# Kernel tuning notes

Hardware: AMD Instinct MI355X
Metric: run time of the kernel (lower is better)

The kernel has to match this reference:

```python
import jax, jax.numpy as jnp
import numpy as np

DIM = 128
CODEBOOK_SIZE = 1024


def setup_inputs() -> dict:
    key = jax.random.key(0)
    kx, ke = jax.random.split(key)
    x = jax.random.normal(kx, (16, 4096, DIM), dtype=jnp.float32)
    # kaiming_uniform_ on (codebook_size, dim): bound = sqrt(6 / fan_in), fan_in = dim
    bound = float(np.sqrt(6.0 / DIM))
    embed = jax.random.uniform(ke, (CODEBOOK_SIZE, DIM), dtype=jnp.float32,
                               minval=-bound, maxval=bound)
    return {"x": x, "embed": embed}


def reference(x, embed):
    orig_shape = x.shape
    flat = x.reshape(-1, x.shape[-1])                     # [N, D]
    x2 = jnp.sum(flat * flat, axis=1, keepdims=True)      # [N, 1]
    e2 = jnp.sum(embed * embed, axis=1)                   # [K]
    dist = -(x2 - 2.0 * (flat @ embed.T) + e2[None, :])   # [N, K]
    embed_ind = jnp.argmax(dist, axis=-1)                 # [N]
    embed_ind = embed_ind.reshape(orig_shape[:-1])        # [B, S]
    quantize = jnp.take(embed, embed_ind, axis=0)         # [B, S, D]
    return quantize, embed_ind
```

## Files before the change

kernel.cpp:

```cpp
#include <hip/hip_runtime.h>

#define DIM     128
#define NCODES  1024
#define TILE_M  64
#define FLAGThr 0.018f
#define RPB     4
#define RGRID   1024

typedef __attribute__((ext_vector_type(8))) _Float16 half8;
typedef __attribute__((ext_vector_type(4))) _Float16 half4;
typedef __attribute__((ext_vector_type(4))) float    f32x4;

#define AS1 __attribute__((address_space(1)))
#define AS3 __attribute__((address_space(3)))


__global__ __launch_bounds__(256) void setup_kernel(
    const float* __restrict__ embed, double* __restrict__ e2d,
    float* __restrict__ e2f, _Float16* __restrict__ eh,
    float* __restrict__ embedT, int* __restrict__ cnt)
{
  __shared__ float tile[64][132];
  __shared__ double psum[4][64];
  if (blockIdx.x == 0 && threadIdx.x == 0) *cnt = 0;
  const int c0 = blockIdx.x * 64;
  const int t  = threadIdx.x;

  const f32x4* E4 = (const f32x4*)(embed + (size_t)c0 * DIM);
  #pragma unroll
  for (int i = 0; i < 8; ++i) {
    int e = t + i * 256;
    int r = e >> 5, c4 = e & 31;
    f32x4 v = E4[e];
    *(f32x4*)&tile[r][c4 * 4] = v;
    half4 h;
    h[0] = (_Float16)v[0]; h[1] = (_Float16)v[1];
    h[2] = (_Float16)v[2]; h[3] = (_Float16)v[3];
    *(half4*)&eh[(size_t)(c0 + r) * DIM + c4 * 4] = h;
  }
  __syncthreads();

  {
    int r = t & 63, part = t >> 6;
    double s = 0.0;
    #pragma unroll
    for (int k = 0; k < 32; ++k) {
      float v = tile[r][part * 32 + k];
      s += (double)v * v;
    }
    psum[part][r] = s;
  }
  __syncthreads();
  if (t < 64) {
    double s = psum[0][t] + psum[1][t] + psum[2][t] + psum[3][t];
    e2d[c0 + t] = s;
    e2f[c0 + t] = (float)s;
  }

  #pragma unroll
  for (int i = 0; i < 32; ++i) {
    int idx = t + i * 256;
    int k = idx >> 6, c = idx & 63;
    embedT[(size_t)k * NCODES + c0 + c] = tile[c][k];
  }
}

__global__ __launch_bounds__(256, 3) void pass1_kernel(
    const float* __restrict__ x, const float* __restrict__ embed,
    const _Float16* __restrict__ eh, const float* __restrict__ e2f,
    float* __restrict__ outQ, float* __restrict__ outIdx,
    int* __restrict__ cnt, int* __restrict__ list)
{
  __shared__ __align__(16) _Float16 xh[TILE_M * 136];
  __shared__ __align__(16) unsigned char bbuf[2][64 * 256];
  __shared__ float rb_best[4][TILE_M];
  __shared__ float rb_sec [4][TILE_M];
  __shared__ int   fidx[TILE_M];

  const int tid  = threadIdx.x;
  const int row0 = blockIdx.x * TILE_M;
  const int l  = tid & 63, w = tid >> 6;
  const int rl = l & 15,  q = l >> 4;

#define STAGE_B(CH, BUF)                                                      \
  {                                                                           \
    const char* ebase = (const char*)eh + (size_t)(CH) * 64 * 256;            \
    _Pragma("unroll")                                                         \
    for (int j = 0; j < 4; ++j) {                                             \
      int u  = (w * 4 + j) * 64 + l;              \
      int rr = u >> 4, cc = u & 15;                                           \
      const char* src = ebase + rr * 256 + ((cc ^ (rr & 15)) * 16);           \
      __builtin_amdgcn_global_load_lds(                                       \
          (AS1 void*)src,                                                     \
          (AS3 void*)((BUF) + (w * 4 + j) * 1024), 16, 0, 0);                 \
    }                                                                         \
  }

  {
    const f32x4* x4 = (const f32x4*)(x + (size_t)row0 * DIM);
    #pragma unroll
    for (int i = 0; i < 8; ++i) {
      int e = tid + i * 256;
      int r = e >> 5, c4 = e & 31;
      f32x4 v = x4[e];
      half4 h;
      h[0] = (_Float16)v[0]; h[1] = (_Float16)v[1];
      h[2] = (_Float16)v[2]; h[3] = (_Float16)v[3];
      *(half4*)&xh[r * 136 + c4 * 4] = h;
    }
  }
  STAGE_B(0, bbuf[0])
  __syncthreads();

  half8 afrag[4][4];
  #pragma unroll
  for (int m = 0; m < 4; ++m)
    #pragma unroll
    for (int ks = 0; ks < 4; ++ks)
      afrag[m][ks] = *(const half8*)&xh[(m * 16 + rl) * 136 + ks * 32 + q * 8];

  float bestp[16], secp[16];
  #pragma unroll
  for (int s = 0; s < 16; ++s) { bestp[s] = -3.0e38f; secp[s] = -3.3e38f; }

  #pragma unroll
  for (int ch = 0; ch < 16; ++ch) {
    if (ch < 15) STAGE_B(ch + 1, bbuf[(ch + 1) & 1])
    const unsigned char* bb = bbuf[ch & 1];
    half8 bfrag[4];
    #pragma unroll
    for (int ks = 0; ks < 4; ++ks)
      bfrag[ks] = *(const half8*)(bb + (w * 16 + rl) * 256 +
                                  (((ks * 4 + q) ^ rl) * 16));
    const float vinit = fmaf(-0.5f, e2f[ch * 64 + w * 16 + rl], -16.0f);
    const int mycode = ch * 64 + w * 16 + rl;
    #pragma unroll
    for (int m = 0; m < 4; ++m) {
      f32x4 acc = (f32x4){vinit, vinit, vinit, vinit};
      #pragma unroll
      for (int ks = 0; ks < 4; ++ks)
        acc = __builtin_amdgcn_mfma_f32_16x16x32_f16(afrag[m][ks], bfrag[ks], acc, 0, 0, 0);
      #pragma unroll
      for (int r = 0; r < 4; ++r) {
        const int s = m * 4 + r;
        float scp = __int_as_float((__float_as_int(acc[r]) & ~1023) | mycode);
        secp[s]  = __builtin_amdgcn_fmed3f(scp, bestp[s], secp[s]);
        bestp[s] = fmaxf(bestp[s], scp);
      }
    }
    __syncthreads();
  }
#undef STAGE_B

  #pragma unroll
  for (int off = 1; off < 16; off <<= 1) {
    #pragma unroll
    for (int s = 0; s < 16; ++s) {
      float ob = __shfl_xor(bestp[s], off, 16);
      float os = __shfl_xor(secp[s],  off, 16);
      secp[s]  = fmaxf(__builtin_amdgcn_fmed3f(bestp[s], ob, secp[s]), os);
      bestp[s] = fmaxf(bestp[s], ob);
    }
  }
  if (rl == 0) {
    #pragma unroll
    for (int m = 0; m < 4; ++m)
      #pragma unroll
      for (int r = 0; r < 4; ++r) {
        int s = m * 4 + r;
        int row = m * 16 + q * 4 + r;
        rb_best[w][row] = bestp[s];
        rb_sec [w][row] = secp[s];
      }
  }
  __syncthreads();

  if (tid < TILE_M) {
    float bv = rb_best[0][tid], sv = rb_sec[0][tid];
    #pragma unroll
    for (int ww = 1; ww < 4; ++ww) {
      float ob = rb_best[ww][tid], os = rb_sec[ww][tid];
      sv = fmaxf(__builtin_amdgcn_fmed3f(bv, ob, sv), os);
      bv = fmaxf(bv, ob);
    }
    int bi = __float_as_int(bv) & 1023;
    int grow = row0 + tid;
    outIdx[grow] = (float)bi;
    fidx[tid] = bi;
    if (bv - sv <= FLAGThr) {
      int p = atomicAdd(cnt, 1);
      list[p] = grow;
    }
  }
  __syncthreads();

  {
    const f32x4* E4   = (const f32x4*)embed;
    f32x4*       out4 = (f32x4*)(outQ + (size_t)row0 * DIM);
    #pragma unroll
    for (int i = 0; i < 8; ++i) {
      int e = tid + i * 256;
      int r = e >> 5, c4 = e & 31;
      out4[e] = E4[fidx[r] * 32 + c4];
    }
  }
}

__global__ __launch_bounds__(256) void refine2_kernel(
    const float* __restrict__ x, const float* __restrict__ embed,
    const float* __restrict__ embedT,
    const double* __restrict__ e2d, const float* __restrict__ e2f,
    float* __restrict__ outQ, float* __restrict__ outIdx,
    const int* __restrict__ cnt, const int* __restrict__ list)
{
  __shared__ f32x4 xst[DIM];
  __shared__ float rb1[RPB][4], rb2[RPB][4];
  __shared__ int   ri1[RPB][4], ri2[RPB][4];
  __shared__ int   cand[RPB][2];

  const int t = threadIdx.x;
  const int l = t & 63, w = t >> 6;
  const int n = *cnt;
  float* xsf = (float*)xst;

  for (int base = blockIdx.x * RPB; base < n; base += RGRID * RPB) {
    const int nr = min(RPB, n - base);
    #pragma unroll
    for (int i = 0; i < 2; ++i) {
      int idx = t + i * 256;
      int r = idx >> 7, k = idx & 127;
      float v = 0.f;
      if (r < nr) v = x[(size_t)list[base + r] * DIM + k];
      xsf[k * RPB + r] = v;
    }
    __syncthreads();

    f32x4 dot[RPB];
    #pragma unroll
    for (int r = 0; r < RPB; ++r) dot[r] = (f32x4){0.f, 0.f, 0.f, 0.f};
    const f32x4* eT4 = (const f32x4*)embedT;
    #pragma unroll 4
    for (int k = 0; k < DIM; ++k) {
      f32x4 e4  = eT4[k * 256 + t];
      f32x4 xk4 = xst[k];
      #pragma unroll
      for (int r = 0; r < RPB; ++r) {
        dot[r][0] = fmaf(xk4[r], e4[0], dot[r][0]);
        dot[r][1] = fmaf(xk4[r], e4[1], dot[r][1]);
        dot[r][2] = fmaf(xk4[r], e4[2], dot[r][2]);
        dot[r][3] = fmaf(xk4[r], e4[3], dot[r][3]);
      }
    }

    #pragma unroll
    for (int r = 0; r < RPB; ++r) {
      float b1 = 3.4e38f, b2 = 3.4e38f; int i1 = 0, i2 = 0;
      #pragma unroll
      for (int j = 0; j < 4; ++j) {
        int c = 4 * t + j;
        float sc = fmaf(-2.0f, dot[r][j], e2f[c]);
        bool better = (sc < b1);
        float lv = better ? b1 : sc;  int li = better ? i1 : c;
        if (better) { b1 = sc; i1 = c; }
        bool t2 = (lv < b2) || (lv == b2 && li < i2);
        if (t2) { b2 = lv; i2 = li; }
      }
      #pragma unroll
      for (int off = 1; off < 64; off <<= 1) {
        float o1 = __shfl_xor(b1, off, 64); int oi1 = __shfl_xor(i1, off, 64);
        float o2 = __shfl_xor(b2, off, 64); int oi2 = __shfl_xor(i2, off, 64);
        bool take = (o1 < b1) || (o1 == b1 && oi1 < i1);
        float n1 = take ? o1 : b1; int ni1 = take ? oi1 : i1;
        float lo = take ? b1 : o1; int loi = take ? i1 : oi1;
        float c2v = take ? o2 : b2; int c2i = take ? oi2 : i2;
        bool u2 = (c2v < lo) || (c2v == lo && c2i < loi);
        b1 = n1; i1 = ni1;
        b2 = u2 ? c2v : lo; i2 = u2 ? c2i : loi;
      }
      if (l == 0) { rb1[r][w] = b1; ri1[r][w] = i1; rb2[r][w] = b2; ri2[r][w] = i2; }
    }
    __syncthreads();

    if (t < RPB) {
      float v1 = rb1[t][0], v2 = rb2[t][0]; int j1 = ri1[t][0], j2 = ri2[t][0];
      #pragma unroll
      for (int ww = 1; ww < 4; ++ww) {
        float o1 = rb1[t][ww], o2 = rb2[t][ww]; int oi1 = ri1[t][ww], oi2 = ri2[t][ww];
        bool take = (o1 < v1) || (o1 == v1 && oi1 < j1);
        float n1 = take ? o1 : v1; int ni1 = take ? oi1 : j1;
        float lo = take ? v1 : o1; int loi = take ? j1 : oi1;
        float c2v = take ? o2 : v2; int c2i = take ? oi2 : j2;
        bool u2 = (c2v < lo) || (c2v == lo && c2i < loi);
        v1 = n1; j1 = ni1; v2 = u2 ? c2v : lo; j2 = u2 ? c2i : loi;
      }
      cand[t][0] = j1; cand[t][1] = j2;
    }
    __syncthreads();

    if (w < nr) {
      int c1 = cand[w][0], c2 = cand[w][1];
      float xa = xsf[l * RPB + w], xb = xsf[(l + 64) * RPB + w];
      double p1 = (double)xa * (double)embed[(size_t)c1 * DIM + l]
                + (double)xb * (double)embed[(size_t)c1 * DIM + 64 + l];
      double p2 = (double)xa * (double)embed[(size_t)c2 * DIM + l]
                + (double)xb * (double)embed[(size_t)c2 * DIM + 64 + l];
      #pragma unroll
      for (int off = 1; off < 64; off <<= 1) {
        p1 += __shfl_xor(p1, off, 64);
        p2 += __shfl_xor(p2, off, 64);
      }
      double s1 = e2d[c1] - 2.0 * p1;
      double s2 = e2d[c2] - 2.0 * p2;
      int widx = ((s2 < s1) || (s2 == s1 && c2 < c1)) ? c2 : c1;
      int row = list[base + w];
      if (l == 0) outIdx[row] = (float)widx;
      outQ[(size_t)row * DIM + l]      = embed[(size_t)widx * DIM + l];
      outQ[(size_t)row * DIM + 64 + l] = embed[(size_t)widx * DIM + 64 + l];
    }
    __syncthreads();
  }
}

extern "C" void kernel_launch(void* const* d_in, const int* in_sizes, int n_in,
                              void* d_out, int out_size, void* d_ws, size_t ws_size,
                              hipStream_t stream) {
  const float* x     = (const float*)d_in[0];
  const float* embed = (const float*)d_in[1];
  const int N = in_sizes[0] / DIM;

  float* out    = (float*)d_out;
  float* outQ   = out;
  float* outIdx = out + (size_t)N * DIM;

  char* ws = (char*)d_ws;
  double*   e2d  = (double*)  (ws);
  float*    e2f  = (float*)   (ws + 8192);
  _Float16* eh   = (_Float16*)(ws + 12288);
  float*    eT   = (float*)   (ws + 274432);
  int*      cnt  = (int*)     (ws + 798720);
  int*      list = (int*)     (ws + 798976);

  setup_kernel  <<<NCODES / 64, 256, 0, stream>>>(embed, e2d, e2f, eh, eT, cnt);
  pass1_kernel  <<<N / TILE_M,  256, 0, stream>>>(x, embed, eh, e2f, outQ, outIdx, cnt, list);
  refine2_kernel<<<RGRID,       256, 0, stream>>>(x, embed, eT, e2d, e2f, outQ, outIdx, cnt, list);
}
```

Before: 151.3 us.

## Triple-buffer codebook chunks with prefetch depth two and a single barrier per chunk

The shared-memory double buffer for codebook chunks becomes a triple buffer carved from one raw LDS array, and chunks are now prefetched two ahead using explicit vmcnt waits instead of a full __syncthreads. The per-chunk codebook norm loads are hoisted into a 16-entry register array before the loop. This aims to hide global-to-LDS latency and drop one barrier per chunk. In exchange it uses more LDS and registers, which may cut occupancy under the 3-blocks-per-SM launch bound, and it relies on hand-written waitcnt counts being correct.

```diff
diff --git a/kernel.cpp b/kernel.cpp
--- a/kernel.cpp
+++ b/kernel.cpp
@@ -71,20 +71,23 @@
     float* __restrict__ outQ, float* __restrict__ outIdx,
     int* __restrict__ cnt, int* __restrict__ list)
 {
-  __shared__ __align__(16) _Float16 xh[TILE_M * 136];
-  __shared__ __align__(16) unsigned char bbuf[2][64 * 256];
-  __shared__ float rb_best[4][TILE_M];
-  __shared__ float rb_sec [4][TILE_M];
-  __shared__ int   fidx[TILE_M];
+  __shared__ __align__(16) unsigned char smem[52480];
+  _Float16* xh = (_Float16*)smem;
+  float (*rb_best)[TILE_M] = (float (*)[TILE_M])(smem + 50176);
+  float (*rb_sec )[TILE_M] = (float (*)[TILE_M])(smem + 51200);
+  int*   fidx              = (int*)  (smem + 52224);
 
   const int tid  = threadIdx.x;
   const int row0 = blockIdx.x * TILE_M;
   const int l  = tid & 63, w = tid >> 6;
   const int rl = l & 15,  q = l >> 4;
 
-#define STAGE_B(CH, BUF)                                                      \
+  constexpr int BOFF[3] = {17408, 33792, 0};
+
+#define STAGE_B(CH)                                                           \
   {                                                                           \
     const char* ebase = (const char*)eh + (size_t)(CH) * 64 * 256;            \
+    unsigned char* buf = smem + BOFF[(CH) % 3];                               \
     _Pragma("unroll")                                                         \
     for (int j = 0; j < 4; ++j) {                                             \
       int u  = (w * 4 + j) * 64 + l;              \
@@ -92,9 +95,14 @@
       const char* src = ebase + rr * 256 + ((cc ^ (rr & 15)) * 16);           \
       __builtin_amdgcn_global_load_lds(                                       \
           (AS1 void*)src,                                                     \
-          (AS3 void*)((BUF) + (w * 4 + j) * 1024), 16, 0, 0);                 \
+          (AS3 void*)(buf + (w * 4 + j) * 1024), 16, 0, 0);                   \
     }                                                                         \
   }
+
+  float vin[16];
+  #pragma unroll
+  for (int g = 0; g < 16; ++g)
+    vin[g] = fmaf(-0.5f, e2f[g * 64 + w * 16 + rl], -16.0f);
 
   {
     const f32x4* x4 = (const f32x4*)(x + (size_t)row0 * DIM);
@@ -109,8 +117,10 @@
       *(half4*)&xh[r * 136 + c4 * 4] = h;
     }
   }
-  STAGE_B(0, bbuf[0])
-  __syncthreads();
+  STAGE_B(0)
+  STAGE_B(1)
+  asm volatile("s_waitcnt lgkmcnt(0)" ::: "memory");
+  __builtin_amdgcn_s_barrier();
 
   half8 afrag[4][4];
   #pragma unroll
@@ -125,14 +135,21 @@
 
   #pragma unroll
   for (int ch = 0; ch < 16; ++ch) {
-    if (ch < 15) STAGE_B(ch + 1, bbuf[(ch + 1) & 1])
-    const unsigned char* bb = bbuf[ch & 1];
+    if (ch < 15) {
+      asm volatile("s_waitcnt vmcnt(4) lgkmcnt(0)" ::: "memory");
+    } else {
+      asm volatile("s_waitcnt vmcnt(0) lgkmcnt(0)" ::: "memory");
+    }
+    __builtin_amdgcn_s_barrier();
+    if (ch + 2 < 16) STAGE_B(ch + 2)
+
+    const unsigned char* bb = smem + BOFF[ch % 3];
     half8 bfrag[4];
     #pragma unroll
     for (int ks = 0; ks < 4; ++ks)
       bfrag[ks] = *(const half8*)(bb + (w * 16 + rl) * 256 +
                                   (((ks * 4 + q) ^ rl) * 16));
-    const float vinit = fmaf(-0.5f, e2f[ch * 64 + w * 16 + rl], -16.0f);
+    const float vinit = vin[ch];
     const int mycode = ch * 64 + w * 16 + rl;
     #pragma unroll
     for (int m = 0; m < 4; ++m) {
@@ -148,7 +165,6 @@
         bestp[s] = fmaxf(bestp[s], scp);
       }
     }
-    __syncthreads();
   }
 #undef STAGE_B
 
@@ -162,6 +178,7 @@
       bestp[s] = fmaxf(bestp[s], ob);
     }
   }
+  __syncthreads();
   if (rl == 0) {
     #pragma unroll
     for (int m = 0; m < 4; ++m)
```

Result: slower. 176.6 us (+16.8%).

## Use per-wave private codebook buffers to drop block barriers in pass1 loop

Applied to the files above, without the earlier changes.

Each wave now stages only its own 16 codebook rows into a private double buffer, with two chunks in flight, and waits with explicit vmcnt/lgkmcnt counters instead of a block-wide __syncthreads per chunk. The per-chunk e2 bias values are preloaded into registers before the loop. This removes 16 workgroup barriers and lets waves progress independently, at the cost of extra registers for the bias values and reliance on hand-tuned waitcnt correctness.

```diff
diff --git a/kernel.cpp b/kernel.cpp
--- a/kernel.cpp
+++ b/kernel.cpp
@@ -72,7 +72,7 @@
     int* __restrict__ cnt, int* __restrict__ list)
 {
   __shared__ __align__(16) _Float16 xh[TILE_M * 136];
-  __shared__ __align__(16) unsigned char bbuf[2][64 * 256];
+  __shared__ __align__(16) unsigned char bbuf[4][2][4096];
   __shared__ float rb_best[4][TILE_M];
   __shared__ float rb_sec [4][TILE_M];
   __shared__ int   fidx[TILE_M];
@@ -82,19 +82,25 @@
   const int l  = tid & 63, w = tid >> 6;
   const int rl = l & 15,  q = l >> 4;
 
-#define STAGE_B(CH, BUF)                                                      \
+#define STAGE_W(CH)                                                           \
   {                                                                           \
-    const char* ebase = (const char*)eh + (size_t)(CH) * 64 * 256;            \
+    const char* ebase = (const char*)eh + ((size_t)(CH) * 64 + w * 16) * 256; \
+    unsigned char* buf = bbuf[w][(CH) & 1];                                   \
     _Pragma("unroll")                                                         \
     for (int j = 0; j < 4; ++j) {                                             \
-      int u  = (w * 4 + j) * 64 + l;              \
+      int u  = j * 64 + l;                   \
       int rr = u >> 4, cc = u & 15;                                           \
-      const char* src = ebase + rr * 256 + ((cc ^ (rr & 15)) * 16);           \
+      const char* src = ebase + rr * 256 + ((cc ^ rr) * 16);                  \
       __builtin_amdgcn_global_load_lds(                                       \
           (AS1 void*)src,                                                     \
-          (AS3 void*)((BUF) + (w * 4 + j) * 1024), 16, 0, 0);                 \
+          (AS3 void*)(buf + j * 1024), 16, 0, 0);                             \
     }                                                                         \
   }
+
+  float vin[16];
+  #pragma unroll
+  for (int g = 0; g < 16; ++g)
+    vin[g] = fmaf(-0.5f, e2f[g * 64 + w * 16 + rl], -16.0f);
 
   {
     const f32x4* x4 = (const f32x4*)(x + (size_t)row0 * DIM);
@@ -109,7 +115,6 @@
       *(half4*)&xh[r * 136 + c4 * 4] = h;
     }
   }
-  STAGE_B(0, bbuf[0])
   __syncthreads();
 
   half8 afrag[4][4];
@@ -123,16 +128,25 @@
   #pragma unroll
   for (int s = 0; s < 16; ++s) { bestp[s] = -3.0e38f; secp[s] = -3.3e38f; }
 
+  STAGE_W(0)
+  STAGE_W(1)
+
   #pragma unroll
   for (int ch = 0; ch < 16; ++ch) {
-    if (ch < 15) STAGE_B(ch + 1, bbuf[(ch + 1) & 1])
-    const unsigned char* bb = bbuf[ch & 1];
+    if (ch < 15) {
+      asm volatile("s_waitcnt vmcnt(4)" ::: "memory");
+    } else {
+      asm volatile("s_waitcnt vmcnt(0)" ::: "memory");
+    }
+    __builtin_amdgcn_sched_barrier(0);
+
+    const unsigned char* bb = bbuf[w][ch & 1];
     half8 bfrag[4];
     #pragma unroll
     for (int ks = 0; ks < 4; ++ks)
-      bfrag[ks] = *(const half8*)(bb + (w * 16 + rl) * 256 +
-                                  (((ks * 4 + q) ^ rl) * 16));
-    const float vinit = fmaf(-0.5f, e2f[ch * 64 + w * 16 + rl], -16.0f);
+      bfrag[ks] = *(const half8*)(bb + rl * 256 + (((ks * 4 + q) ^ rl) * 16));
+
+    const float vinit = vin[ch];
     const int mycode = ch * 64 + w * 16 + rl;
     #pragma unroll
     for (int m = 0; m < 4; ++m) {
@@ -148,9 +162,14 @@
         bestp[s] = fmaxf(bestp[s], scp);
       }
     }
-    __syncthreads();
-  }
-#undef STAGE_B
+
+    if (ch + 2 < 16) {
+      asm volatile("s_waitcnt lgkmcnt(0)" ::: "memory");
+      __builtin_amdgcn_sched_barrier(0);
+      STAGE_W(ch + 2)
+    }
+  }
+#undef STAGE_W
 
   #pragma unroll
   for (int off = 1; off < 16; off <<= 1) {
```

After: 137.5 us. 9.1% less time.
